# Kernel tuning notes

Measured on AMD Instinct MI355X. Metric: run time of the kernel, lower is better.

## Reference

```python
import jax, jax.numpy as jnp
import numpy as np

N_NODES = 100000
N_EDGES = 1600000
IN_CH, HID_CH, OUT_CH = 128, 128, 64


def _glorot(key, shape):
    lim = np.sqrt(6.0 / (shape[0] + shape[1])).astype(np.float32)
    return jax.random.uniform(key, shape, jnp.float32, -lim, lim)


def setup_inputs() -> dict:
    key = jax.random.key(0)
    ks = jax.random.split(key, 11)
    x = jax.random.normal(ks[0], (N_NODES, IN_CH), jnp.float32)
    edge_index = jax.random.randint(ks[1], (2, N_EDGES), 0, N_NODES, dtype=jnp.int64)
    dims = [(IN_CH, HID_CH), (HID_CH, HID_CH), (HID_CH, OUT_CH)]
    params = {}
    for i, (din, dout) in enumerate(dims):
        params[f"Wl{i}"] = _glorot(ks[2 + 3 * i], (din, dout))
        params[f"Wr{i}"] = _glorot(ks[3 + 3 * i], (din, dout))
        params[f"b{i}"] = jnp.zeros((dout,), jnp.float32)
    return {"x": x, "edge_index": edge_index, **params}


def _sage_conv(x, src, dst, Wl, Wr, b):
    # mean aggregation of neighbor (source) features at each destination node
    msg_sum = jax.ops.segment_sum(x[src], dst, num_segments=N_NODES)  # [N, din]
    deg = jax.ops.segment_sum(jnp.ones((src.shape[0],), x.dtype), dst,
                              num_segments=N_NODES)
    mean = msg_sum / jnp.maximum(deg, 1.0)[:, None]
    # lin_l(aggr) + lin_r(self), bias only in lin_l (PyG SAGEConv default)
    return mean @ Wl + x @ Wr + b


def reference(x, edge_index, Wl0, Wr0, b0, Wl1, Wr1, b1, Wl2, Wr2, b2):
    src, dst = edge_index[0], edge_index[1]
    h = jax.nn.relu(_sage_conv(x, src, dst, Wl0, Wr0, b0))  # dropout = identity (eval)
    h = jax.nn.relu(_sage_conv(h, src, dst, Wl1, Wr1, b1))
    out = _sage_conv(h, src, dst, Wl2, Wr2, b2)
    return out
```

## Files before the change

kernel.cpp:

```cpp
#include <hip/hip_runtime.h>
#include <stdint.h>

#define NN 100000
#define NE 1600000
#define NBUK 782
#define G 256
#define CHUNK 6250

typedef unsigned int u32;
typedef unsigned short u16;
typedef short v8s __attribute__((ext_vector_type(8)));
typedef float v4f __attribute__((ext_vector_type(4)));

union U4S8 {
    uint4 u;
    v8s s;
};

__device__ __forceinline__ float bf2f(u16 u) {
    return __uint_as_float(((u32)u) << 16);
}
__device__ __forceinline__ u16 f2bf(float f) {
    u32 u = __float_as_uint(f);
    u = u + 0x7FFFu + ((u >> 16) & 1u);
    return (u16)(u >> 16);
}
__device__ __forceinline__ float lo16(u32 u) { return __uint_as_float(u << 16); }
__device__ __forceinline__ float hi16(u32 u) {
    return __uint_as_float(u & 0xFFFF0000u);
}

__global__ void detect_kernel(const u32* __restrict__ ei,
                              const u32* __restrict__ x, int* flags) {
    __shared__ int bad64, badbf;
    int t = threadIdx.x;
    if (t == 0) { bad64 = 0; badbf = 0; }
    __syncthreads();
    if (ei[2 * t + 1] != 0u) atomicAdd(&bad64, 1);
    u32 d = x[t];
    u32 e = (d >> 7) & 0xFFu;
    if (e != 0u && (e < 96u || e > 160u)) atomicAdd(&badbf, 1);
    __syncthreads();
    if (t == 0) {
        flags[0] = (bad64 < 16) ? 1 : 0;
        flags[1] = (badbf < 16) ? 1 : 0;
    }
}

__global__ void conv_x(const void* __restrict__ x, const int* __restrict__ flags,
                       u32* __restrict__ xb, u32* __restrict__ h1,
                       u32* __restrict__ h2) {
    int i = blockIdx.x * 256 + threadIdx.x;
    if (i >= NN * 64) {
        int p = i - NN * 64;
        if (p < 64) {
            xb[NN * 64 + p] = 0;
            h1[NN * 64 + p] = 0;
            h2[NN * 64 + p] = 0;
        }
        return;
    }
    u32 o;
    if (flags[1]) {
        o = ((const u32*)x)[i];
    } else {
        float2 v = ((const float2*)x)[i];
        o = ((u32)f2bf(v.y) << 16) | (u32)f2bf(v.x);
    }
    xb[i] = o;
}

__global__ void wt_prep_all(const void* __restrict__ Wr0,
                            const void* __restrict__ Wl0,
                            const void* __restrict__ b0,
                            const void* __restrict__ Wr1,
                            const void* __restrict__ Wl1,
                            const void* __restrict__ b1,
                            const void* __restrict__ Wr2,
                            const void* __restrict__ Wl2,
                            const void* __restrict__ b2,
                            const int* __restrict__ flags,
                            u16* __restrict__ WT0, float* __restrict__ bf0,
                            u16* __restrict__ WT1, float* __restrict__ bf1,
                            u16* __restrict__ WT2, float* __restrict__ bf2_) {
    const void* Wr;
    const void* Wl;
    const void* bias;
    u16* WT;
    float* bias_f;
    int cout, t;
    if (blockIdx.x < 128) {
        Wr = Wr0; Wl = Wl0; bias = b0; WT = WT0; bias_f = bf0; cout = 128;
        t = blockIdx.x * 256 + threadIdx.x;
    } else if (blockIdx.x < 256) {
        Wr = Wr1; Wl = Wl1; bias = b1; WT = WT1; bias_f = bf1; cout = 128;
        t = (blockIdx.x - 128) * 256 + threadIdx.x;
    } else {
        Wr = Wr2; Wl = Wl2; bias = b2; WT = WT2; bias_f = bf2_; cout = 64;
        t = (blockIdx.x - 256) * 256 + threadIdx.x;
    }
    if (t < 256 * cout) {
        int k = t / cout, c = t % cout;
        const void* W = (k < 128) ? Wr : Wl;
        int kk = k & 127;
        float v;
        if (flags[1])
            v = bf2f(((const u16*)W)[kk * cout + c]);
        else
            v = ((const float*)W)[kk * cout + c];
        WT[c * 256 + k] = f2bf(v);
    }
    if (t < cout) {
        bias_f[t] =
            flags[1] ? bf2f(((const u16*)bias)[t]) : ((const float*)bias)[t];
    }
}

__global__ __launch_bounds__(256) void p1_hist(const void* __restrict__ ei,
                                               const int* __restrict__ flags,
                                               int* __restrict__ hist) {
    __shared__ int h[NBUK];
    int g = blockIdx.x, t = threadIdx.x;
    for (int b = t; b < NBUK; b += 256) h[b] = 0;
    __syncthreads();
    int e0 = g * CHUNK;
    int e1 = e0 + CHUNK;
    const int* p = (const int*)ei;
    if (flags[0]) {
        for (int e = e0 + t; e < e1; e += 256)
            atomicAdd(&h[p[2 * (NE + e)] >> 7], 1);
    } else {
        for (int e = e0 + t; e < e1; e += 256)
            atomicAdd(&h[p[NE + e] >> 7], 1);
    }
    __syncthreads();
    for (int b = t; b < NBUK; b += 256) hist[b * G + g] = h[b];
}

__global__ void scan_block_g(const int* __restrict__ in, int* __restrict__ out,
                             int* __restrict__ bsums, int n) {
    __shared__ int sS[256];
    int t = threadIdx.x;
    int base = blockIdx.x * 1024 + t * 4;
    int c[4];
#pragma unroll
    for (int i = 0; i < 4; ++i) c[i] = (base + i < n) ? in[base + i] : 0;
    int s = c[0] + c[1] + c[2] + c[3];
    sS[t] = s;
    __syncthreads();
    for (int dlt = 1; dlt < 256; dlt <<= 1) {
        int v = (t >= dlt) ? sS[t - dlt] : 0;
        __syncthreads();
        sS[t] += v;
        __syncthreads();
    }
    int run = sS[t] - s;
    if (t == 255) bsums[blockIdx.x] = sS[255];
#pragma unroll
    for (int i = 0; i < 4; ++i) {
        if (base + i < n) out[base + i] = run;
        run += c[i];
    }
}

__global__ void scan_top_g(int* bsums, int nb) {
    __shared__ int sS[256];
    int t = threadIdx.x;
    int v = (t < nb) ? bsums[t] : 0;
    sS[t] = v;
    __syncthreads();
    for (int d = 1; d < 256; d <<= 1) {
        int u = (t >= d) ? sS[t - d] : 0;
        __syncthreads();
        sS[t] += u;
        __syncthreads();
    }
    if (t < nb) bsums[t] = sS[t] - v;
}

__global__ void scan_add_g(int* __restrict__ out, const int* __restrict__ bsums,
                           int n) {
    int i = blockIdx.x * 256 + threadIdx.x;
    if (i < n) out[i] += bsums[i >> 10];
}

__global__ __launch_bounds__(256) void p2_scatter(const void* __restrict__ ei,
                                                  const int* __restrict__ flags,
                                                  const int* __restrict__ histS,
                                                  int2* __restrict__ ebuf) {
    __shared__ int cur[NBUK];
    int g = blockIdx.x, t = threadIdx.x;
    for (int b = t; b < NBUK; b += 256) cur[b] = histS[b * G + g];
    __syncthreads();
    int e0 = g * CHUNK;
    int e1 = e0 + CHUNK;
    const int* p = (const int*)ei;
    int is64 = flags[0];
    for (int e = e0 + t; e < e1; e += 256) {
        int s, d;
        if (is64) {
            s = p[2 * e];
            d = p[2 * (NE + e)];
        } else {
            s = p[e];
            d = p[NE + e];
        }
        int pos = atomicAdd(&cur[d >> 7], 1);
        ebuf[pos] = make_int2(s, d);
    }
}

__global__ __launch_bounds__(256) void p3_build(const int* __restrict__ histS,
                                                const int2* __restrict__ ebuf,
                                                int* __restrict__ off,
                                                int* __restrict__ ssrc) {
    __shared__ int cnt[128], pref[128], cur[128];
    int b = blockIdx.x, t = threadIdx.x;
    int node0 = b << 7;
    int bs = histS[b * G];
    int be = (b == NBUK - 1) ? NE : histS[(b + 1) * G];
    if (t < 128) cnt[t] = 0;
    __syncthreads();
    for (int e = bs + t; e < be; e += 256)
        atomicAdd(&cnt[ebuf[e].y - node0], 1);
    __syncthreads();
    if (t < 128) pref[t] = cnt[t];
    __syncthreads();
    for (int d = 1; d < 128; d <<= 1) {
        int v = 0;
        if (t < 128 && t >= d) v = pref[t - d];
        __syncthreads();
        if (t < 128) pref[t] += v;
        __syncthreads();
    }
    if (t < 128) {
        int ex = pref[t] - cnt[t];
        cur[t] = ex;
        int node = node0 + t;
        if (node < NN) off[node] = bs + ex;
    }
    if (b == NBUK - 1 && t == 0) off[NN] = NE;
    __syncthreads();
    for (int e = bs + t; e < be; e += 256) {
        int2 sd = ebuf[e];
        int pos = atomicAdd(&cur[sd.y - node0], 1);
        ssrc[bs + pos] = sd.x;
    }
}

__global__ __launch_bounds__(256) void gather_mean_b(
    const u32* __restrict__ feat, const int* __restrict__ off,
    const int* __restrict__ ssrc, u32* __restrict__ meanB) {
    int node = blockIdx.x * 4 + (threadIdx.x >> 6);
    int lane = threadIdx.x & 63;
    int o0 = __builtin_amdgcn_readfirstlane(off[node]);
    int o1 = __builtin_amdgcn_readfirstlane(off[node + 1]);
    int cnt = o1 - o0;
    float a0 = 0.f, a1 = 0.f;
    for (int base = 0; base < cnt; base += 64) {
        int lim = cnt - base;
        if (lim > 64) lim = 64;
        int myidx = (lane < lim) ? ssrc[o0 + base + lane] : NN;
        int jb = (lim + 15) & ~15;
        for (int j = 0; j < jb; j += 16) {
            u32 uu[16];
#pragma unroll
            for (int q = 0; q < 16; ++q) {
                int sidx = __builtin_amdgcn_readlane(myidx, j + q);
                uu[q] = feat[(size_t)sidx * 64 + lane];
            }
#pragma unroll
            for (int q = 0; q < 16; ++q) {
                a0 += lo16(uu[q]);
                a1 += hi16(uu[q]);
            }
        }
    }
    float inv = 1.0f / (float)(cnt > 0 ? cnt : 1);
    meanB[node * 64 + lane] =
        ((u32)f2bf(a1 * inv) << 16) | (u32)f2bf(a0 * inv);
}

template <int COUT, bool RELU, bool FINAL>
__global__ __launch_bounds__(256, 2) void sage_mfma(
    const u16* __restrict__ selfB, const u16* __restrict__ meanB,
    const u16* __restrict__ WT, const float* __restrict__ bias_f,
    void* __restrict__ out, const int* __restrict__ flags) {
    constexpr int CT = COUT / 16;
    __shared__ u16 wlds[256 * COUT];
    const int tid = threadIdx.x;
    const int wave = tid >> 6;
    const int lane = tid & 63;
    const int n16 = lane & 15;
    const int quad = lane >> 4;
    const int bfin = flags[1];

    {
        const uint4* src = (const uint4*)WT;
        char* wb = (char*)wlds;
        constexpr int NITER = (COUT * 32) / 256;
#pragma unroll
        for (int i = 0; i < NITER; ++i) {
            int idx = i * 256 + tid;
            int c = idx >> 5;
            int off = (idx & 31) << 4;
            *(uint4*)(wb + c * 512 + (off ^ ((c & 7) << 4))) = src[idx];
        }
    }
    __syncthreads();

    const int rowb = blockIdx.x * 256 + wave * 64 + n16;
    int rr[4];
#pragma unroll
    for (int mt = 0; mt < 4; ++mt) {
        int r = rowb + mt * 16;
        r = (r < NN) ? r : (NN - 1);
        rr[mt] = r * 128 + quad * 8;
    }

    v4f acc[4][CT];
#pragma unroll
    for (int mt = 0; mt < 4; ++mt)
#pragma unroll
        for (int ct = 0; ct < CT; ++ct) acc[mt][ct] = (v4f)(0.f);

    const char* wb = (const char*)wlds;
    const int swz = (n16 & 7) << 4;
#pragma unroll
    for (int ks = 0; ks < 8; ++ks) {
        const int ko = (ks & 3) * 32;
        const u16* bp = (ks < 4) ? selfB : meanB;
        U4S8 nf[4];
#pragma unroll
        for (int mt = 0; mt < 4; ++mt)
            nf[mt].u = *(const uint4*)(bp + rr[mt] + ko);
        U4S8 wf[CT];
#pragma unroll
        for (int ct = 0; ct < CT; ++ct) {
            int addr = (ct * 16 + n16) * 512 + ((ks * 64 + quad * 16) ^ swz);
            wf[ct].u = *(const uint4*)(wb + addr);
        }
#pragma unroll
        for (int mt = 0; mt < 4; ++mt)
#pragma unroll
            for (int ct = 0; ct < CT; ++ct)
                acc[mt][ct] = __builtin_amdgcn_mfma_f32_16x16x32_bf16(
                    wf[ct].s, nf[mt].s, acc[mt][ct], 0, 0, 0);
    }

    float4 bv[CT];
#pragma unroll
    for (int ct = 0; ct < CT; ++ct)
        bv[ct] = *(const float4*)&bias_f[ct * 16 + quad * 4];

#pragma unroll
    for (int mt = 0; mt < 4; ++mt) {
        int row = rowb + mt * 16;
        if (row < NN) {
#pragma unroll
            for (int ct = 0; ct < CT; ++ct) {
                float v0 = acc[mt][ct][0] + bv[ct].x;
                float v1 = acc[mt][ct][1] + bv[ct].y;
                float v2 = acc[mt][ct][2] + bv[ct].z;
                float v3 = acc[mt][ct][3] + bv[ct].w;
                if (RELU) {
                    v0 = fmaxf(v0, 0.f);
                    v1 = fmaxf(v1, 0.f);
                    v2 = fmaxf(v2, 0.f);
                    v3 = fmaxf(v3, 0.f);
                }
                if (FINAL && !bfin) {
                    float4 o = {v0, v1, v2, v3};
                    *(float4*)((float*)out + (size_t)row * COUT + ct * 16 +
                               quad * 4) = o;
                } else {
                    uint2 o;
                    o.x = (u32)f2bf(v0) | ((u32)f2bf(v1) << 16);
                    o.y = (u32)f2bf(v2) | ((u32)f2bf(v3) << 16);
                    *(uint2*)((u16*)out + (size_t)row * COUT + ct * 16 +
                              quad * 4) = o;
                }
            }
        }
    }
}

extern "C" void kernel_launch(void* const* d_in, const int* in_sizes, int n_in,
                              void* d_out, int out_size, void* d_ws,
                              size_t ws_size, hipStream_t stream) {
    const void* x = d_in[0];
    const void* ei = d_in[1];
    const void* Wl0 = d_in[2];
    const void* Wr0 = d_in[3];
    const void* b0 = d_in[4];
    const void* Wl1 = d_in[5];
    const void* Wr1 = d_in[6];
    const void* b1 = d_in[7];
    const void* Wl2 = d_in[8];
    const void* Wr2 = d_in[9];
    const void* b2 = d_in[10];

    char* ws = (char*)d_ws;
    size_t o = 0;
    auto alloc = [&](size_t bytes) {
        void* p = ws + o;
        o = (o + bytes + 511) & ~(size_t)511;
        return p;
    };
    int* flags = (int*)alloc(16);
    int* hist = (int*)alloc((size_t)NBUK * G * 4);
    int* bsums = (int*)alloc(256 * 4);
    int* off = (int*)alloc((NN + 1) * 4);
    int* ssrc = (int*)alloc((size_t)NE * 4);
    int2* ebuf = (int2*)alloc((size_t)NE * 8);
    u32* xb = (u32*)alloc((size_t)(NN + 1) * 64 * 4);
    u32* meanB = (u32*)alloc((size_t)NN * 64 * 4);
    u32* h1 = (u32*)alloc((size_t)(NN + 1) * 64 * 4);
    u32* h2 = (u32*)alloc((size_t)(NN + 1) * 64 * 4);
    u16* WT0 = (u16*)alloc(256 * 128 * 2);
    u16* WT1 = (u16*)alloc(256 * 128 * 2);
    u16* WT2 = (u16*)alloc(256 * 64 * 2);
    float* bf0 = (float*)alloc(128 * 4);
    float* bf1 = (float*)alloc(128 * 4);
    float* bf2_ = (float*)alloc(64 * 4);

    constexpr int L = NBUK * G;
    constexpr int NBLK = (L + 1023) / 1024;
    constexpr int RB = (NN + 255) / 256;

    detect_kernel<<<1, 256, 0, stream>>>((const u32*)ei, (const u32*)x, flags);
    conv_x<<<(NN * 64 + 64 + 255) / 256, 256, 0, stream>>>(x, flags, xb, h1,
                                                           h2);
    wt_prep_all<<<320, 256, 0, stream>>>(Wr0, Wl0, b0, Wr1, Wl1, b1, Wr2, Wl2,
                                         b2, flags, WT0, bf0, WT1, bf1, WT2,
                                         bf2_);

    p1_hist<<<G, 256, 0, stream>>>(ei, flags, hist);
    scan_block_g<<<NBLK, 256, 0, stream>>>(hist, hist, bsums, L);
    scan_top_g<<<1, 256, 0, stream>>>(bsums, NBLK);
    scan_add_g<<<(L + 255) / 256, 256, 0, stream>>>(hist, bsums, L);
    p2_scatter<<<G, 256, 0, stream>>>(ei, flags, hist, ebuf);
    p3_build<<<NBUK, 256, 0, stream>>>(hist, ebuf, off, ssrc);

    gather_mean_b<<<NN / 4, 256, 0, stream>>>(xb, off, ssrc, meanB);
    sage_mfma<128, true, false><<<RB, 256, 0, stream>>>(
        (const u16*)xb, (const u16*)meanB, WT0, bf0, h1, flags);
    gather_mean_b<<<NN / 4, 256, 0, stream>>>(h1, off, ssrc, meanB);
    sage_mfma<128, true, false><<<RB, 256, 0, stream>>>(
        (const u16*)h1, (const u16*)meanB, WT1, bf1, h2, flags);
    gather_mean_b<<<NN / 4, 256, 0, stream>>>(h2, off, ssrc, meanB);
    sage_mfma<64, false, true><<<RB, 256, 0, stream>>>(
        (const u16*)h2, (const u16*)meanB, WT2, bf2_, d_out, flags);
}
```

Before: 399.5 us.

## Split feature matrices into per-16-channel slabs so each XCD gathers an L2-sized slab

Node features are stored as eight column-group slabs of 16 bf16 channels each, with a zero padding row per slab. The gather kernel assigns column group `blockIdx & 7` to each block, so with round-robin block dispatch each XCD should touch only one slab of about 3.2 MB, which can stay resident in its L2. Each wave now processes 8 edges at once with 8 lanes per row and combines lanes with a shuffle reduction. The MFMA kernel's input addressing and its non-final output stores are changed to read and write the slab layout. The trade-off is fewer outstanding loads per wave than the old 16-deep unrolled gather, plus extra shuffle work per node.

```diff
diff --git a/kernel.cpp b/kernel.cpp
--- a/kernel.cpp
+++ b/kernel.cpp
@@ -30,6 +30,8 @@
     return __uint_as_float(u & 0xFFFF0000u);
 }
 
+#define SL ((NN + 1) * 8)
+
 __global__ void detect_kernel(const u32* __restrict__ ei,
                               const u32* __restrict__ x, int* flags) {
     __shared__ int bad64, badbf;
@@ -48,26 +50,29 @@
 }
 
 __global__ void conv_x(const void* __restrict__ x, const int* __restrict__ flags,
-                       u32* __restrict__ xb, u32* __restrict__ h1,
-                       u32* __restrict__ h2) {
+                       u32* __restrict__ xbG, u32* __restrict__ h1G,
+                       u32* __restrict__ h2G) {
     int i = blockIdx.x * 256 + threadIdx.x;
-    if (i >= NN * 64) {
-        int p = i - NN * 64;
-        if (p < 64) {
-            xb[NN * 64 + p] = 0;
-            h1[NN * 64 + p] = 0;
-            h2[NN * 64 + p] = 0;
-        }
+    if (i >= (NN + 1) * 64) return;
+    int c = i & 7;
+    int q = i >> 3;
+    int node = q % (NN + 1);
+    int g = q / (NN + 1);
+    if (node == NN) {
+        xbG[i] = 0;
+        h1G[i] = 0;
+        h2G[i] = 0;
         return;
     }
+    int col = g * 8 + c;
     u32 o;
     if (flags[1]) {
-        o = ((const u32*)x)[i];
+        o = ((const u32*)x)[node * 64 + col];
     } else {
-        float2 v = ((const float2*)x)[i];
+        float2 v = ((const float2*)x)[node * 64 + col];
         o = ((u32)f2bf(v.y) << 16) | (u32)f2bf(v.x);
     }
-    xb[i] = o;
+    xbG[i] = o;
 }
 
 __global__ void wt_prep_all(const void* __restrict__ Wr0,
@@ -248,42 +253,61 @@
     }
 }
 
-__global__ __launch_bounds__(256) void gather_mean_b(
-    const u32* __restrict__ feat, const int* __restrict__ off,
-    const int* __restrict__ ssrc, u32* __restrict__ meanB) {
-    int node = blockIdx.x * 4 + (threadIdx.x >> 6);
-    int lane = threadIdx.x & 63;
-    int o0 = __builtin_amdgcn_readfirstlane(off[node]);
-    int o1 = __builtin_amdgcn_readfirstlane(off[node + 1]);
-    int cnt = o1 - o0;
-    float a0 = 0.f, a1 = 0.f;
-    for (int base = 0; base < cnt; base += 64) {
-        int lim = cnt - base;
-        if (lim > 64) lim = 64;
-        int myidx = (lane < lim) ? ssrc[o0 + base + lane] : NN;
-        int jb = (lim + 15) & ~15;
-        for (int j = 0; j < jb; j += 16) {
-            u32 uu[16];
-#pragma unroll
-            for (int q = 0; q < 16; ++q) {
-                int sidx = __builtin_amdgcn_readlane(myidx, j + q);
-                uu[q] = feat[(size_t)sidx * 64 + lane];
-            }
-#pragma unroll
-            for (int q = 0; q < 16; ++q) {
-                a0 += lo16(uu[q]);
-                a1 += hi16(uu[q]);
-            }
-        }
-    }
-    float inv = 1.0f / (float)(cnt > 0 ? cnt : 1);
-    meanB[node * 64 + lane] =
-        ((u32)f2bf(a1 * inv) << 16) | (u32)f2bf(a0 * inv);
+__global__ __launch_bounds__(256) void gather_mean_g(
+    const u32* __restrict__ featG, const int* __restrict__ off,
+    const int* __restrict__ ssrc, u32* __restrict__ meanG) {
+    const int g = blockIdx.x & 7;
+    const int nb = blockIdx.x >> 3;
+    const int wave = threadIdx.x >> 6;
+    const int lane = threadIdx.x & 63;
+    const int e = lane >> 3;
+    const int c = lane & 7;
+    const u32* fg = featG + (size_t)g * SL;
+    u32* mg = meanG + (size_t)g * SL;
+    const int node0 = nb * 32 + wave * 8;
+    for (int node = node0; node < node0 + 8; ++node) {
+        int o0 = __builtin_amdgcn_readfirstlane(off[node]);
+        int o1 = __builtin_amdgcn_readfirstlane(off[node + 1]);
+        int cnt = o1 - o0;
+        float a0 = 0.f, a1 = 0.f;
+        int full = cnt & ~15;
+        int base = 0;
+        for (; base < full; base += 16) {
+            int i0 = ssrc[o0 + base + e];
+            int i1 = ssrc[o0 + base + 8 + e];
+            u32 u0 = fg[i0 * 8 + c];
+            u32 u1 = fg[i1 * 8 + c];
+            a0 += lo16(u0);
+            a1 += hi16(u0);
+            a0 += lo16(u1);
+            a1 += hi16(u1);
+        }
+        if (base < cnt) {
+            int s0 = base + e, s1 = base + 8 + e;
+            int i0 = (s0 < cnt) ? ssrc[o0 + s0] : NN;
+            int i1 = (s1 < cnt) ? ssrc[o0 + s1] : NN;
+            u32 u0 = fg[i0 * 8 + c];
+            u32 u1 = fg[i1 * 8 + c];
+            a0 += lo16(u0);
+            a1 += hi16(u0);
+            a0 += lo16(u1);
+            a1 += hi16(u1);
+        }
+#pragma unroll
+        for (int m = 8; m <= 32; m <<= 1) {
+            a0 += __shfl_xor(a0, m, 64);
+            a1 += __shfl_xor(a1, m, 64);
+        }
+        float inv = 1.0f / (float)(cnt > 0 ? cnt : 1);
+        if (lane < 8)
+            mg[(size_t)node * 8 + lane] =
+                ((u32)f2bf(a1 * inv) << 16) | (u32)f2bf(a0 * inv);
+    }
 }
 
 template <int COUT, bool RELU, bool FINAL>
 __global__ __launch_bounds__(256, 2) void sage_mfma(
-    const u16* __restrict__ selfB, const u16* __restrict__ meanB,
+    const u32* __restrict__ selfG, const u32* __restrict__ meanG,
     const u16* __restrict__ WT, const float* __restrict__ bias_f,
     void* __restrict__ out, const int* __restrict__ flags) {
     constexpr int CT = COUT / 16;
@@ -310,12 +334,14 @@
     __syncthreads();
 
     const int rowb = blockIdx.x * 256 + wave * 64 + n16;
-    int rr[4];
+    const int gq = quad >> 1;
+    const int wcol = (quad & 1) * 4;
+    int rbase[4];
 #pragma unroll
     for (int mt = 0; mt < 4; ++mt) {
         int r = rowb + mt * 16;
         r = (r < NN) ? r : (NN - 1);
-        rr[mt] = r * 128 + quad * 8;
+        rbase[mt] = r * 8 + gq * SL + wcol;
     }
 
     v4f acc[4][CT];
@@ -328,12 +354,12 @@
     const int swz = (n16 & 7) << 4;
 #pragma unroll
     for (int ks = 0; ks < 8; ++ks) {
-        const int ko = (ks & 3) * 32;
-        const u16* bp = (ks < 4) ? selfB : meanB;
+        const u32* bp = (ks < 4) ? selfG : meanG;
+        const int kof = (ks & 3) * 2 * SL;
         U4S8 nf[4];
 #pragma unroll
         for (int mt = 0; mt < 4; ++mt)
-            nf[mt].u = *(const uint4*)(bp + rr[mt] + ko);
+            nf[mt].u = *(const uint4*)(bp + kof + rbase[mt]);
         U4S8 wf[CT];
 #pragma unroll
         for (int ct = 0; ct < CT; ++ct) {
@@ -377,8 +403,13 @@
                     uint2 o;
                     o.x = (u32)f2bf(v0) | ((u32)f2bf(v1) << 16);
                     o.y = (u32)f2bf(v2) | ((u32)f2bf(v3) << 16);
-                    *(uint2*)((u16*)out + (size_t)row * COUT + ct * 16 +
-                              quad * 4) = o;
+                    if (FINAL) {
+                        *(uint2*)((u16*)out + (size_t)row * COUT + ct * 16 +
+                                  quad * 4) = o;
+                    } else {
+                        *(uint2*)((u32*)out + (size_t)ct * SL + (size_t)row * 8 +
+                                  quad * 2) = o;
+                    }
                 }
             }
         }
@@ -414,7 +445,7 @@
     int* ssrc = (int*)alloc((size_t)NE * 4);
     int2* ebuf = (int2*)alloc((size_t)NE * 8);
     u32* xb = (u32*)alloc((size_t)(NN + 1) * 64 * 4);
-    u32* meanB = (u32*)alloc((size_t)NN * 64 * 4);
+    u32* meanB = (u32*)alloc((size_t)(NN + 1) * 64 * 4);
     u32* h1 = (u32*)alloc((size_t)(NN + 1) * 64 * 4);
     u32* h2 = (u32*)alloc((size_t)(NN + 1) * 64 * 4);
     u16* WT0 = (u16*)alloc(256 * 128 * 2);
@@ -427,10 +458,11 @@
     constexpr int L = NBUK * G;
     constexpr int NBLK = (L + 1023) / 1024;
     constexpr int RB = (NN + 255) / 256;
+    constexpr int GB = 8 * (NN / 32);
 
     detect_kernel<<<1, 256, 0, stream>>>((const u32*)ei, (const u32*)x, flags);
-    conv_x<<<(NN * 64 + 64 + 255) / 256, 256, 0, stream>>>(x, flags, xb, h1,
-                                                           h2);
+    conv_x<<<((NN + 1) * 64 + 255) / 256, 256, 0, stream>>>(x, flags, xb, h1,
+                                                            h2);
     wt_prep_all<<<320, 256, 0, stream>>>(Wr0, Wl0, b0, Wr1, Wl1, b1, Wr2, Wl2,
                                          b2, flags, WT0, bf0, WT1, bf1, WT2,
                                          bf2_);
@@ -442,13 +474,13 @@
     p2_scatter<<<G, 256, 0, stream>>>(ei, flags, hist, ebuf);
     p3_build<<<NBUK, 256, 0, stream>>>(hist, ebuf, off, ssrc);
 
-    gather_mean_b<<<NN / 4, 256, 0, stream>>>(xb, off, ssrc, meanB);
-    sage_mfma<128, true, false><<<RB, 256, 0, stream>>>(
-        (const u16*)xb, (const u16*)meanB, WT0, bf0, h1, flags);
-    gather_mean_b<<<NN / 4, 256, 0, stream>>>(h1, off, ssrc, meanB);
-    sage_mfma<128, true, false><<<RB, 256, 0, stream>>>(
-        (const u16*)h1, (const u16*)meanB, WT1, bf1, h2, flags);
-    gather_mean_b<<<NN / 4, 256, 0, stream>>>(h2, off, ssrc, meanB);
-    sage_mfma<64, false, true><<<RB, 256, 0, stream>>>(
-        (const u16*)h2, (const u16*)meanB, WT2, bf2_, d_out, flags);
-}
+    gather_mean_g<<<GB, 256, 0, stream>>>(xb, off, ssrc, meanB);
+    sage_mfma<128, true, false><<<RB, 256, 0, stream>>>(xb, meanB, WT0, bf0,
+                                                        h1, flags);
+    gather_mean_g<<<GB, 256, 0, stream>>>(h1, off, ssrc, meanB);
+    sage_mfma<128, true, false><<<RB, 256, 0, stream>>>(h1, meanB, WT1, bf1,
+                                                        h2, flags);
+    gather_mean_g<<<GB, 256, 0, stream>>>(h2, off, ssrc, meanB);
+    sage_mfma<64, false, true><<<RB, 256, 0, stream>>>(h2, meanB, WT2, bf2_,
+                                                       d_out, flags);
+}
```

After: 677.7 us. 69.6% more time.
